# Optimization experiments

Measured on AMD Instinct MI355X. Metric: run time of the kernel, lower is better.

## Reference

```python
import jax, jax.numpy as jnp
import numpy as np
import math

B, S, E, H = 4, 2048, 1024, 16
HD = E // H


def _linear_params(key, out_dim, in_dim):
    k1, k2 = jax.random.split(key)
    W = jax.random.normal(k1, (out_dim, in_dim), dtype=jnp.float32) * 0.02
    b = jax.random.normal(k2, (out_dim,), dtype=jnp.float32) * 0.02
    return W, b


def setup_inputs() -> dict:
    key = jax.random.key(0)
    ks = jax.random.split(key, 12)
    query = jax.random.normal(ks[0], (B, S, E), dtype=jnp.float32)
    k_in = jax.random.normal(ks[1], (B, S, E), dtype=jnp.float32)
    v_in = jax.random.normal(ks[2], (B, S, E), dtype=jnp.float32)
    uncertainty = jax.random.uniform(ks[3], (B, 1, 1), dtype=jnp.float32)
    key_padding_mask = jnp.zeros((B, S), dtype=bool)
    Wq, bq = _linear_params(ks[4], E, E)
    Wk, bk = _linear_params(ks[5], E, E)
    Wv, bv = _linear_params(ks[6], E, E)
    Wuq, buq = _linear_params(ks[7], E, 1)
    Wuk, buk = _linear_params(ks[8], E, 1)
    Wo, bo = _linear_params(ks[9], E, E)
    Wg, bg = _linear_params(ks[10], 1, E)
    return {
        'query': query, 'key': k_in, 'value': v_in,
        'uncertainty': uncertainty, 'key_padding_mask': key_padding_mask,
        'Wq': Wq, 'bq': bq, 'Wk': Wk, 'bk': bk, 'Wv': Wv, 'bv': bv,
        'Wuq': Wuq, 'buq': buq, 'Wuk': Wuk, 'buk': buk,
        'Wo': Wo, 'bo': bo, 'Wg': Wg, 'bg': bg,
    }


def reference(query, key, value, uncertainty, key_padding_mask,
              Wq, bq, Wk, bk, Wv, bv, Wuq, buq, Wuk, buk, Wo, bo, Wg, bg):
    Bq, Sq, Eq = query.shape
    scale = 1.0 / math.sqrt(HD)
    # projections -> (B, H, S, HD)
    q = (query @ Wq.T + bq).reshape(Bq, Sq, H, HD).transpose(0, 2, 1, 3)
    k = (key @ Wk.T + bk).reshape(Bq, Sq, H, HD).transpose(0, 2, 1, 3)
    v = (value @ Wv.T + bv).reshape(Bq, Sq, H, HD).transpose(0, 2, 1, 3)
    scores = jnp.einsum('bhqd,bhkd->bhqk', q, k) * scale  # (B,H,S,S)
    # uncertainty bias: per-(batch, head) scalar added to all scores
    unc_q = (uncertainty @ Wuq.T + buq).reshape(Bq, 1, H, HD).transpose(0, 2, 1, 3)  # (B,H,1,HD)
    unc_k = (uncertainty @ Wuk.T + buk).reshape(Bq, 1, H, HD).transpose(0, 2, 1, 3)
    unc_scores = jnp.einsum('bhqd,bhkd->bhqk', unc_q, unc_k) * scale  # (B,H,1,1)
    scores = scores + unc_scores
    scores = jnp.where(key_padding_mask[:, None, None, :], -jnp.inf, scores)
    attn = jax.nn.softmax(scores, axis=-1)  # dropout is identity in eval mode
    attended = jnp.einsum('bhqk,bhkd->bhqd', attn, v)
    attended = attended.transpose(0, 2, 1, 3).reshape(Bq, Sq, Eq)
    output = attended @ Wo.T + bo
    gate = jax.nn.sigmoid(output @ Wg.T + bg)  # (B,S,1)
    output = gate * output + (1.0 - gate) * query
    return output, attn
```

## Files before the change

kernel.cpp:

```cpp
#include <hip/hip_runtime.h>
#include <hip/hip_bf16.h>
#include <math.h>

#define NB 4
#define NS 2048
#define NE 1024
#define NH 16
#define ND 64
#define NBS (NB*NS)

using short8 = __attribute__((ext_vector_type(8))) short;
using short4_t = __attribute__((ext_vector_type(4))) short;
using f32x4  = __attribute__((ext_vector_type(4))) float;

__device__ __forceinline__ short f2bf(float f) {
    union { float f; unsigned u; } v; v.f = f;
    unsigned r = v.u + 0x7FFFu + ((v.u >> 16) & 1u);
    return (short)(r >> 16);
}

__device__ __forceinline__ void gload16(const short* g, short* l) {
    __builtin_amdgcn_global_load_lds(
        (const __attribute__((address_space(1))) void*)g,
        (__attribute__((address_space(3))) void*)l,
        16, 0, 0);
}

__global__ void cvt_kernel(const float* __restrict__ src, short* __restrict__ dst, int n4) {
    int i = blockIdx.x * blockDim.x + threadIdx.x;
    if (i >= n4) return;
    float4 v = reinterpret_cast<const float4*>(src)[i];
    short4_t o;
    o[0] = f2bf(v.x); o[1] = f2bf(v.y); o[2] = f2bf(v.z); o[3] = f2bf(v.w);
    reinterpret_cast<short4_t*>(dst)[i] = o;
}

template<int MODE>
__global__ void gemm_bf16(const short* __restrict__ A, const short* __restrict__ W,
                          const float* __restrict__ bias, void* __restrict__ Cout)
{
    __shared__ short Alds[128 * 64];
    __shared__ short Blds[128 * 64];
    const int t = threadIdx.x;
    const int wid = t >> 6, lane = t & 63, lg = lane >> 4, lr = lane & 15;
    const int wm = wid >> 1, wn = wid & 1;
    const int m0 = blockIdx.y * 128, n0 = blockIdx.x * 128;

    f32x4 acc[4][4];
    #pragma unroll
    for (int ni = 0; ni < 4; ++ni) {
        float bv = bias[n0 + wn*64 + ni*16 + lr];
        #pragma unroll
        for (int mi = 0; mi < 4; ++mi) acc[mi][ni] = f32x4{bv, bv, bv, bv};
    }

    const int grow = wid*32 + (lane >> 3);
    const int gcol = (lane & 7) * 8;

    for (int k0 = 0; k0 < NE; k0 += 64) {
        __syncthreads();
        {
            const short* ap = A + (size_t)(m0 + grow)*NE + k0 + gcol;
            short* lp = Alds + wid*2048 + lane*8;
            #pragma unroll
            for (int c = 0; c < 4; ++c)
                gload16(ap + (size_t)c*8*NE, lp + c*512);
        }
        {
            const short* bp = W + (size_t)(n0 + grow)*NE + k0 + gcol;
            short* lp = Blds + wid*2048 + lane*8;
            #pragma unroll
            for (int c = 0; c < 4; ++c)
                gload16(bp + (size_t)c*8*NE, lp + c*512);
        }
        __syncthreads();
        #pragma unroll
        for (int ks = 0; ks < 2; ++ks) {
            short8 af[4], bfr[4];
            #pragma unroll
            for (int mi = 0; mi < 4; ++mi)
                af[mi] = *(const short8*)&Alds[(wm*64 + mi*16 + lr)*64 + ks*32 + lg*8];
            #pragma unroll
            for (int ni = 0; ni < 4; ++ni)
                bfr[ni] = *(const short8*)&Blds[(wn*64 + ni*16 + lr)*64 + ks*32 + lg*8];
            #pragma unroll
            for (int mi = 0; mi < 4; ++mi)
                #pragma unroll
                for (int ni = 0; ni < 4; ++ni)
                    acc[mi][ni] = __builtin_amdgcn_mfma_f32_16x16x32_bf16(af[mi], bfr[ni], acc[mi][ni], 0, 0, 0);
        }
    }

    #pragma unroll
    for (int mi = 0; mi < 4; ++mi) {
        #pragma unroll
        for (int ni = 0; ni < 4; ++ni) {
            #pragma unroll
            for (int j = 0; j < 4; ++j) {
                int m = m0 + wm*64 + mi*16 + lg*4 + j;
                int n = n0 + wn*64 + ni*16 + lr;
                int b = m >> 11, s = m & 2047;
                int h = n >> 6,  d = n & 63;
                int bh = b*NH + h;
                if (MODE == 0) {
                    ((short*)Cout)[((size_t)bh*NS + s)*ND + d] = f2bf(acc[mi][ni][j]);
                } else if (MODE == 1) {
                    ((float*)Cout)[(size_t)m*NE + n] = acc[mi][ni][j];
                } else if (MODE == 2) {
                    size_t base = ((size_t)(bh*32 + (s >> 6))*64 + (s & 63)) * 64;
                    int scol = (((d >> 3) ^ (s & 7)) << 3) + (d & 7);
                    ((short*)Cout)[base + scol] = f2bf(acc[mi][ni][j]);
                } else {
                    size_t base = ((size_t)(bh*32 + (s >> 6))*64 + d) * 64;
                    int scol = ((((s >> 3) & 7) ^ (d & 7)) << 3) + (s & 7);
                    ((short*)Cout)[base + scol] = f2bf(acc[mi][ni][j]);
                }
            }
        }
    }
}

__global__ __launch_bounds__(256, 3)
void attn_kernel(const short* __restrict__ Qb, const short* __restrict__ Kt,
                 const short* __restrict__ Vt, float* __restrict__ attn_out,
                 short* __restrict__ attended)
{
    __shared__ short Klds[2][64*64];
    __shared__ short Vlds[2][64*64];
    __shared__ short Plds[4][16][72];

    const int qb = blockIdx.x;
    const int bh = blockIdx.y;
    const int b = bh >> 4, h = bh & 15;
    const int t = threadIdx.x;
    const int wid = t >> 6, lane = t & 63, lg = lane >> 4, lr = lane & 15;
    const float scale = 0.125f;

    const short* qrow = Qb + ((size_t)bh*NS + qb*64 + wid*16 + lr)*ND;
    short8 qf0 = *(const short8*)(qrow + lg*8);
    short8 qf1 = *(const short8*)(qrow + 32 + lg*8);

    int fOff[4][2];
    #pragma unroll
    for (int i = 0; i < 4; ++i) {
        int row = i*16 + lr;
        fOff[i][0] = row*128 + ((lg ^ (row & 7)) << 4);
        fOff[i][1] = row*128 + (((lg + 4) ^ (row & 7)) << 4);
    }
    const int stOff = wid*512 + lane*8;
    const short* ktBase = Kt + (size_t)bh*32*4096 + stOff;
    const short* vtBase = Vt + (size_t)bh*32*4096 + stOff;

    gload16(ktBase, &Klds[0][stOff]);
    gload16(ktBase + 2048, &Klds[0][stOff + 2048]);
    __syncthreads();

    float rsum[4] = {0.f, 0.f, 0.f, 0.f};
    for (int t6 = 0; t6 < 32; ++t6) {
        int cur = t6 & 1;
        if (t6 < 31) {
            const short* kp = ktBase + (size_t)(t6 + 1)*4096;
            gload16(kp, &Klds[cur ^ 1][stOff]);
            gload16(kp + 2048, &Klds[cur ^ 1][stOff + 2048]);
        }
        #pragma unroll
        for (int ct = 0; ct < 4; ++ct) {
            short8 kf0 = *(const short8*)((const char*)Klds[cur] + fOff[ct][0]);
            short8 kf1 = *(const short8*)((const char*)Klds[cur] + fOff[ct][1]);
            f32x4 s = f32x4{0.f, 0.f, 0.f, 0.f};
            s = __builtin_amdgcn_mfma_f32_16x16x32_bf16(qf0, kf0, s, 0, 0, 0);
            s = __builtin_amdgcn_mfma_f32_16x16x32_bf16(qf1, kf1, s, 0, 0, 0);
            #pragma unroll
            for (int j = 0; j < 4; ++j) rsum[j] += __expf(s[j] * scale);
        }
        __syncthreads();
    }
    #pragma unroll
    for (int m = 1; m < 16; m <<= 1) {
        #pragma unroll
        for (int j = 0; j < 4; ++j) rsum[j] += __shfl_xor(rsum[j], m, 64);
    }
    float inv[4];
    #pragma unroll
    for (int j = 0; j < 4; ++j) inv[j] = 1.0f / rsum[j];

    size_t rb[4];
    #pragma unroll
    for (int j = 0; j < 4; ++j)
        rb[j] = ((size_t)bh * NS + (size_t)(qb*64 + wid*16 + lg*4 + j)) * NS;

    f32x4 pv[4];
    #pragma unroll
    for (int dt = 0; dt < 4; ++dt) pv[dt] = f32x4{0.f, 0.f, 0.f, 0.f};

    gload16(ktBase, &Klds[0][stOff]);
    gload16(ktBase + 2048, &Klds[0][stOff + 2048]);
    gload16(vtBase, &Vlds[0][stOff]);
    gload16(vtBase + 2048, &Vlds[0][stOff + 2048]);
    __syncthreads();

    for (int t6 = 0; t6 < 32; ++t6) {
        int cur = t6 & 1;
        if (t6 < 31) {
            const short* kp = ktBase + (size_t)(t6 + 1)*4096;
            const short* vp = vtBase + (size_t)(t6 + 1)*4096;
            gload16(kp, &Klds[cur ^ 1][stOff]);
            gload16(kp + 2048, &Klds[cur ^ 1][stOff + 2048]);
            gload16(vp, &Vlds[cur ^ 1][stOff]);
            gload16(vp + 2048, &Vlds[cur ^ 1][stOff + 2048]);
        }
        int kt = t6 * 64;
        #pragma unroll
        for (int ct = 0; ct < 4; ++ct) {
            short8 kf0 = *(const short8*)((const char*)Klds[cur] + fOff[ct][0]);
            short8 kf1 = *(const short8*)((const char*)Klds[cur] + fOff[ct][1]);
            f32x4 s = f32x4{0.f, 0.f, 0.f, 0.f};
            s = __builtin_amdgcn_mfma_f32_16x16x32_bf16(qf0, kf0, s, 0, 0, 0);
            s = __builtin_amdgcn_mfma_f32_16x16x32_bf16(qf1, kf1, s, 0, 0, 0);
            #pragma unroll
            for (int j = 0; j < 4; ++j) {
                float p = __expf(s[j] * scale) * inv[j];
                __builtin_nontemporal_store(p, &attn_out[rb[j] + kt + ct*16 + lr]);
                Plds[wid][lg*4 + j][ct*16 + lr] = f2bf(p);
            }
        }
        short8 pf0 = *(const short8*)&Plds[wid][lr][lg*8];
        short8 pf1 = *(const short8*)&Plds[wid][lr][32 + lg*8];
        #pragma unroll
        for (int dt = 0; dt < 4; ++dt) {
            short8 vf0 = *(const short8*)((const char*)Vlds[cur] + fOff[dt][0]);
            short8 vf1 = *(const short8*)((const char*)Vlds[cur] + fOff[dt][1]);
            pv[dt] = __builtin_amdgcn_mfma_f32_16x16x32_bf16(pf0, vf0, pv[dt], 0, 0, 0);
            pv[dt] = __builtin_amdgcn_mfma_f32_16x16x32_bf16(pf1, vf1, pv[dt], 0, 0, 0);
        }
        __syncthreads();
    }

    #pragma unroll
    for (int dt = 0; dt < 4; ++dt) {
        #pragma unroll
        for (int j = 0; j < 4; ++j) {
            int srow_ = qb*64 + wid*16 + lg*4 + j;
            attended[((size_t)b*NS + srow_)*NE + h*ND + dt*16 + lr] = f2bf(pv[dt][j]);
        }
    }
}

__global__ void gate_kernel(float* __restrict__ out, const float* __restrict__ query,
                            const float* __restrict__ Wg, const float* __restrict__ bg)
{
    __shared__ float red[4];
    const int row = blockIdx.x;
    const int t = threadIdx.x;
    float* orow = out + (size_t)row * NE;
    const float* qrow = query + (size_t)row * NE;

    float4 o = *(float4*)(orow + t*4);
    float4 w = *(const float4*)(Wg + t*4);
    float part = o.x*w.x + o.y*w.y + o.z*w.z + o.w*w.w;
    #pragma unroll
    for (int m = 1; m < 64; m <<= 1) part += __shfl_xor(part, m, 64);
    if ((t & 63) == 0) red[t >> 6] = part;
    __syncthreads();
    float dot = red[0] + red[1] + red[2] + red[3];
    float g = 1.0f / (1.0f + __expf(-(dot + bg[0])));
    float4 q4 = *(const float4*)(qrow + t*4);
    float4 r;
    r.x = g*o.x + (1.0f - g)*q4.x;
    r.y = g*o.y + (1.0f - g)*q4.y;
    r.z = g*o.z + (1.0f - g)*q4.z;
    r.w = g*o.w + (1.0f - g)*q4.w;
    *(float4*)(orow + t*4) = r;
}

extern "C" void kernel_launch(void* const* d_in, const int* in_sizes, int n_in,
                              void* d_out, int out_size, void* d_ws, size_t ws_size,
                              hipStream_t stream) {
    const float* query = (const float*)d_in[0];
    const float* key   = (const float*)d_in[1];
    const float* value = (const float*)d_in[2];
    const float* Wq = (const float*)d_in[5];
    const float* bq = (const float*)d_in[6];
    const float* Wk = (const float*)d_in[7];
    const float* bk = (const float*)d_in[8];
    const float* Wv = (const float*)d_in[9];
    const float* bv = (const float*)d_in[10];
    const float* Wo = (const float*)d_in[15];
    const float* bo = (const float*)d_in[16];
    const float* Wg = (const float*)d_in[17];
    const float* bg = (const float*)d_in[18];

    float* out  = (float*)d_out;
    float* attn = out + (size_t)NBS * NE;

    short* ws = (short*)d_ws;
    const size_t WSZ = (size_t)NE * NE;
    const size_t XSZ = (size_t)NBS * NE;
    short* Wq_b = ws;
    short* Wk_b = Wq_b + WSZ;
    short* Wv_b = Wk_b + WSZ;
    short* Wo_b = Wv_b + WSZ;
    short* Qf   = Wo_b + WSZ;
    short* Kf   = Qf + XSZ;
    short* Vf   = Kf + XSZ;
    short* Qb   = Vf + XSZ;
    short* Kt   = Qb + XSZ;
    short* Vt   = Kt + XSZ;
    short* Att  = Qf;

    cvt_kernel<<<WSZ/1024, 256, 0, stream>>>(Wq, Wq_b, (int)(WSZ/4));
    cvt_kernel<<<WSZ/1024, 256, 0, stream>>>(Wk, Wk_b, (int)(WSZ/4));
    cvt_kernel<<<WSZ/1024, 256, 0, stream>>>(Wv, Wv_b, (int)(WSZ/4));
    cvt_kernel<<<WSZ/1024, 256, 0, stream>>>(Wo, Wo_b, (int)(WSZ/4));
    cvt_kernel<<<XSZ/1024, 256, 0, stream>>>(query, Qf, (int)(XSZ/4));
    cvt_kernel<<<XSZ/1024, 256, 0, stream>>>(key,   Kf, (int)(XSZ/4));
    cvt_kernel<<<XSZ/1024, 256, 0, stream>>>(value, Vf, (int)(XSZ/4));

    dim3 gg(NE/128, NBS/128);
    gemm_bf16<0><<<gg, 256, 0, stream>>>(Qf, Wq_b, bq, Qb);
    gemm_bf16<2><<<gg, 256, 0, stream>>>(Kf, Wk_b, bk, Kt);
    gemm_bf16<3><<<gg, 256, 0, stream>>>(Vf, Wv_b, bv, Vt);

    attn_kernel<<<dim3(NS/64, NB*NH), 256, 0, stream>>>(Qb, Kt, Vt, attn, Att);

    gemm_bf16<1><<<gg, 256, 0, stream>>>(Att, Wo_b, bo, out);

    gate_kernel<<<NBS, 256, 0, stream>>>(out, query, Wg, bg);
}
```

Before: 483.4 us.

## Merge conversion and QKV launches, remap attention grid per XCD, fold normalization

Replaces seven separate fp32-to-bf16 conversion launches with a single kernel covering all weights and activations. The three QKV projection GEMMs are fused into one launch via a selector in the grid's y dimension. The attention grid is flattened and remapped so that blocks sharing a batch-head land on the same XCD for better L2 reuse of K/V. The softmax normalization is folded into the exponent as a log-sum term, removing a multiply per element. Together these cut launch overhead and tail effects, at the cost of slightly different rounding in the probabilities.

```diff
diff --git a/kernel.cpp b/kernel.cpp
--- a/kernel.cpp
+++ b/kernel.cpp
@@ -26,18 +26,122 @@
         16, 0, 0);
 }
 
-__global__ void cvt_kernel(const float* __restrict__ src, short* __restrict__ dst, int n4) {
-    int i = blockIdx.x * blockDim.x + threadIdx.x;
-    if (i >= n4) return;
-    float4 v = reinterpret_cast<const float4*>(src)[i];
+__global__ void cvt_all_kernel(const float* __restrict__ Wq, const float* __restrict__ Wk,
+                               const float* __restrict__ Wv, const float* __restrict__ Wo,
+                               const float* __restrict__ q, const float* __restrict__ k,
+                               const float* __restrict__ v, short* __restrict__ dst)
+{
+    const int i = blockIdx.x * blockDim.x + threadIdx.x;
+    const int W4 = 1 << 18;
+    const int X4 = 1 << 21;
+    const float* src;
+    int off;
+    if (i < 4*W4) {
+        int seg = i >> 18; off = i & (W4 - 1);
+        src = seg == 0 ? Wq : seg == 1 ? Wk : seg == 2 ? Wv : Wo;
+    } else {
+        int j = i - 4*W4;
+        int seg = j >> 21; off = j & (X4 - 1);
+        src = seg == 0 ? q : seg == 1 ? k : v;
+    }
+    float4 val = reinterpret_cast<const float4*>(src)[off];
     short4_t o;
-    o[0] = f2bf(v.x); o[1] = f2bf(v.y); o[2] = f2bf(v.z); o[3] = f2bf(v.w);
+    o[0] = f2bf(val.x); o[1] = f2bf(val.y); o[2] = f2bf(val.z); o[3] = f2bf(val.w);
     reinterpret_cast<short4_t*>(dst)[i] = o;
 }
 
-template<int MODE>
-__global__ void gemm_bf16(const short* __restrict__ A, const short* __restrict__ W,
-                          const float* __restrict__ bias, void* __restrict__ Cout)
+__global__ void qkv_gemm(const short* __restrict__ Abase, const short* __restrict__ Wbase,
+                         const float* __restrict__ bq, const float* __restrict__ bk,
+                         const float* __restrict__ bv, short* __restrict__ Cbase)
+{
+    __shared__ short Alds[128 * 64];
+    __shared__ short Blds[128 * 64];
+    const int t = threadIdx.x;
+    const int wid = t >> 6, lane = t & 63, lg = lane >> 4, lr = lane & 15;
+    const int wm = wid >> 1, wn = wid & 1;
+    const int sel = blockIdx.y >> 6;
+    const int m0 = (blockIdx.y & 63) * 128, n0 = blockIdx.x * 128;
+
+    const short* A = Abase + (size_t)sel * NBS * NE;
+    const short* W = Wbase + (size_t)sel * NE * NE;
+    const float* bias = sel == 0 ? bq : sel == 1 ? bk : bv;
+    short* Cout = Cbase + (size_t)sel * NBS * NE;
+
+    f32x4 acc[4][4];
+    #pragma unroll
+    for (int ni = 0; ni < 4; ++ni) {
+        float bvv = bias[n0 + wn*64 + ni*16 + lr];
+        #pragma unroll
+        for (int mi = 0; mi < 4; ++mi) acc[mi][ni] = f32x4{bvv, bvv, bvv, bvv};
+    }
+
+    const int grow = wid*32 + (lane >> 3);
+    const int gcol = (lane & 7) * 8;
+
+    for (int k0 = 0; k0 < NE; k0 += 64) {
+        __syncthreads();
+        {
+            const short* ap = A + (size_t)(m0 + grow)*NE + k0 + gcol;
+            short* lp = Alds + wid*2048 + lane*8;
+            #pragma unroll
+            for (int c = 0; c < 4; ++c)
+                gload16(ap + (size_t)c*8*NE, lp + c*512);
+        }
+        {
+            const short* bp = W + (size_t)(n0 + grow)*NE + k0 + gcol;
+            short* lp = Blds + wid*2048 + lane*8;
+            #pragma unroll
+            for (int c = 0; c < 4; ++c)
+                gload16(bp + (size_t)c*8*NE, lp + c*512);
+        }
+        __syncthreads();
+        #pragma unroll
+        for (int ks = 0; ks < 2; ++ks) {
+            short8 af[4], bfr[4];
+            #pragma unroll
+            for (int mi = 0; mi < 4; ++mi)
+                af[mi] = *(const short8*)&Alds[(wm*64 + mi*16 + lr)*64 + ks*32 + lg*8];
+            #pragma unroll
+            for (int ni = 0; ni < 4; ++ni)
+                bfr[ni] = *(const short8*)&Blds[(wn*64 + ni*16 + lr)*64 + ks*32 + lg*8];
+            #pragma unroll
+            for (int mi = 0; mi < 4; ++mi)
+                #pragma unroll
+                for (int ni = 0; ni < 4; ++ni)
+                    acc[mi][ni] = __builtin_amdgcn_mfma_f32_16x16x32_bf16(af[mi], bfr[ni], acc[mi][ni], 0, 0, 0);
+        }
+    }
+
+    #pragma unroll
+    for (int mi = 0; mi < 4; ++mi) {
+        #pragma unroll
+        for (int ni = 0; ni < 4; ++ni) {
+            #pragma unroll
+            for (int j = 0; j < 4; ++j) {
+                int m = m0 + wm*64 + mi*16 + lg*4 + j;
+                int n = n0 + wn*64 + ni*16 + lr;
+                int b = m >> 11, s = m & 2047;
+                int h = n >> 6,  d = n & 63;
+                int bh = b*NH + h;
+                short val = f2bf(acc[mi][ni][j]);
+                if (sel == 0) {
+                    Cout[((size_t)bh*NS + s)*ND + d] = val;
+                } else if (sel == 1) {
+                    size_t base = ((size_t)(bh*32 + (s >> 6))*64 + (s & 63)) * 64;
+                    int scol = (((d >> 3) ^ (s & 7)) << 3) + (d & 7);
+                    Cout[base + scol] = val;
+                } else {
+                    size_t base = ((size_t)(bh*32 + (s >> 6))*64 + d) * 64;
+                    int scol = ((((s >> 3) & 7) ^ (d & 7)) << 3) + (s & 7);
+                    Cout[base + scol] = val;
+                }
+            }
+        }
+    }
+}
+
+__global__ void wo_gemm(const short* __restrict__ A, const short* __restrict__ W,
+                        const float* __restrict__ bias, float* __restrict__ Cout)
 {
     __shared__ short Alds[128 * 64];
     __shared__ short Blds[128 * 64];
@@ -92,32 +196,15 @@
     }
 
     #pragma unroll
-    for (int mi = 0; mi < 4; ++mi) {
-        #pragma unroll
-        for (int ni = 0; ni < 4; ++ni) {
+    for (int mi = 0; mi < 4; ++mi)
+        #pragma unroll
+        for (int ni = 0; ni < 4; ++ni)
             #pragma unroll
             for (int j = 0; j < 4; ++j) {
                 int m = m0 + wm*64 + mi*16 + lg*4 + j;
                 int n = n0 + wn*64 + ni*16 + lr;
-                int b = m >> 11, s = m & 2047;
-                int h = n >> 6,  d = n & 63;
-                int bh = b*NH + h;
-                if (MODE == 0) {
-                    ((short*)Cout)[((size_t)bh*NS + s)*ND + d] = f2bf(acc[mi][ni][j]);
-                } else if (MODE == 1) {
-                    ((float*)Cout)[(size_t)m*NE + n] = acc[mi][ni][j];
-                } else if (MODE == 2) {
-                    size_t base = ((size_t)(bh*32 + (s >> 6))*64 + (s & 63)) * 64;
-                    int scol = (((d >> 3) ^ (s & 7)) << 3) + (d & 7);
-                    ((short*)Cout)[base + scol] = f2bf(acc[mi][ni][j]);
-                } else {
-                    size_t base = ((size_t)(bh*32 + (s >> 6))*64 + d) * 64;
-                    int scol = ((((s >> 3) & 7) ^ (d & 7)) << 3) + (s & 7);
-                    ((short*)Cout)[base + scol] = f2bf(acc[mi][ni][j]);
-                }
+                Cout[(size_t)m*NE + n] = acc[mi][ni][j];
             }
-        }
-    }
 }
 
 __global__ __launch_bounds__(256, 3)
@@ -129,8 +216,10 @@
     __shared__ short Vlds[2][64*64];
     __shared__ short Plds[4][16][72];
 
-    const int qb = blockIdx.x;
-    const int bh = blockIdx.y;
+    const int wg = blockIdx.x;
+    const int xcd = wg & 7, slot = wg >> 3;
+    const int bh = xcd*8 + (slot >> 5);
+    const int qb = slot & 31;
     const int b = bh >> 4, h = bh & 15;
     const int t = threadIdx.x;
     const int wid = t >> 6, lane = t & 63, lg = lane >> 4, lr = lane & 15;
@@ -180,9 +269,9 @@
         #pragma unroll
         for (int j = 0; j < 4; ++j) rsum[j] += __shfl_xor(rsum[j], m, 64);
     }
-    float inv[4];
-    #pragma unroll
-    for (int j = 0; j < 4; ++j) inv[j] = 1.0f / rsum[j];
+    float lninv[4];
+    #pragma unroll
+    for (int j = 0; j < 4; ++j) lninv[j] = -__logf(rsum[j]);
 
     size_t rb[4];
     #pragma unroll
@@ -219,7 +308,7 @@
             s = __builtin_amdgcn_mfma_f32_16x16x32_bf16(qf1, kf1, s, 0, 0, 0);
             #pragma unroll
             for (int j = 0; j < 4; ++j) {
-                float p = __expf(s[j] * scale) * inv[j];
+                float p = __expf(fmaf(s[j], scale, lninv[j]));
                 __builtin_nontemporal_store(p, &attn_out[rb[j] + kt + ct*16 + lr]);
                 Plds[wid][lg*4 + j][ct*16 + lr] = f2bf(p);
             }
@@ -237,13 +326,12 @@
     }
 
     #pragma unroll
-    for (int dt = 0; dt < 4; ++dt) {
+    for (int dt = 0; dt < 4; ++dt)
         #pragma unroll
         for (int j = 0; j < 4; ++j) {
             int srow_ = qb*64 + wid*16 + lg*4 + j;
             attended[((size_t)b*NS + srow_)*NE + h*ND + dt*16 + lr] = f2bf(pv[dt][j]);
         }
-    }
 }
 
 __global__ void gate_kernel(float* __restrict__ out, const float* __restrict__ query,
@@ -308,22 +396,13 @@
     short* Vt   = Kt + XSZ;
     short* Att  = Qf;
 
-    cvt_kernel<<<WSZ/1024, 256, 0, stream>>>(Wq, Wq_b, (int)(WSZ/4));
-    cvt_kernel<<<WSZ/1024, 256, 0, stream>>>(Wk, Wk_b, (int)(WSZ/4));
-    cvt_kernel<<<WSZ/1024, 256, 0, stream>>>(Wv, Wv_b, (int)(WSZ/4));
-    cvt_kernel<<<WSZ/1024, 256, 0, stream>>>(Wo, Wo_b, (int)(WSZ/4));
-    cvt_kernel<<<XSZ/1024, 256, 0, stream>>>(query, Qf, (int)(XSZ/4));
-    cvt_kernel<<<XSZ/1024, 256, 0, stream>>>(key,   Kf, (int)(XSZ/4));
-    cvt_kernel<<<XSZ/1024, 256, 0, stream>>>(value, Vf, (int)(XSZ/4));
-
-    dim3 gg(NE/128, NBS/128);
-    gemm_bf16<0><<<gg, 256, 0, stream>>>(Qf, Wq_b, bq, Qb);
-    gemm_bf16<2><<<gg, 256, 0, stream>>>(Kf, Wk_b, bk, Kt);
-    gemm_bf16<3><<<gg, 256, 0, stream>>>(Vf, Wv_b, bv, Vt);
-
-    attn_kernel<<<dim3(NS/64, NB*NH), 256, 0, stream>>>(Qb, Kt, Vt, attn, Att);
-
-    gemm_bf16<1><<<gg, 256, 0, stream>>>(Att, Wo_b, bo, out);
+    cvt_all_kernel<<<28672, 256, 0, stream>>>(Wq, Wk, Wv, Wo, query, key, value, Wq_b);
+
+    qkv_gemm<<<dim3(NE/128, 3*NBS/128), 256, 0, stream>>>(Qf, Wq_b, bq, bk, bv, Qb);
+
+    attn_kernel<<<2048, 256, 0, stream>>>(Qb, Kt, Vt, attn, Att);
+
+    wo_gemm<<<dim3(NE/128, NBS/128), 256, 0, stream>>>(Att, Wo_b, bo, out);
 
     gate_kernel<<<NBS, 256, 0, stream>>>(out, query, Wg, bg);
 }
```

New measurement: 422.5 us (median of 3 runs). 12.6% less time.
